# Performance work log

Measured on AMD Instinct MI355X. Metric: run time of the kernel, lower is better.

The kernel has to match this reference:

```python
import jax, jax.numpy as jnp
import numpy as np

B, L, E, H = 2, 2048, 512, 8
D = E // H  # head_dim = 64


def setup_inputs() -> dict:
    key = jax.random.key(0)
    ks = jax.random.split(key, 12)
    s = 0.02
    return {
        "values": jax.random.normal(ks[0], (B, L, E), jnp.float32),
        "keys": jax.random.normal(ks[1], (B, L, E), jnp.float32),
        "query": jax.random.normal(ks[2], (B, L, E), jnp.float32),
        "mask": jax.random.randint(ks[3], (B, 1, L, L), 0, 2, jnp.int32),
        "Wv": jax.random.normal(ks[4], (E, E), jnp.float32) * s,
        "bv": jax.random.normal(ks[5], (E,), jnp.float32) * s,
        "Wk": jax.random.normal(ks[6], (E, E), jnp.float32) * s,
        "bk": jax.random.normal(ks[7], (E,), jnp.float32) * s,
        "Wq": jax.random.normal(ks[8], (E, E), jnp.float32) * s,
        "bq": jax.random.normal(ks[9], (E,), jnp.float32) * s,
        "Wo": jax.random.normal(ks[10], (E, E), jnp.float32) * s,
        "bo": jax.random.normal(ks[11], (E,), jnp.float32) * s,
    }


def reference(values, keys, query, mask, Wv, bv, Wk, bk, Wq, bq, Wo, bo):
    b, lq = query.shape[0], query.shape[1]
    # torch Linear: y = x @ W.T + b
    v = (values @ Wv.T + bv).reshape(b, -1, H, D)
    k = (keys @ Wk.T + bk).reshape(b, -1, H, D)
    q = (query @ Wq.T + bq).reshape(b, lq, H, D)
    energy = jnp.einsum("bqhd,bkhd->bhqk", q, k)  # [B,H,Lq,Lk]
    # mask applied BEFORE the scale, as in the original
    energy = jnp.where(mask == 0, jnp.float32(-1e20), energy)
    # NOTE: scales by sqrt(embed_size), not sqrt(head_dim) (faithful)
    attn = jax.nn.softmax(energy / jnp.sqrt(jnp.float32(E)), axis=3)
    out = jnp.einsum("bhql,blhd->bqhd", attn, v).reshape(b, lq, E)
    return out @ Wo.T + bo
```

## Files before the change

### kernel.cpp

```cpp
#include <hip/hip_runtime.h>
#include <hip/hip_bf16.h>
#include <math.h>

#define BB 2
#define LL 2048
#define EE 512
#define HH 8
#define DD 64
#define MM (BB * LL)
#define LW (LL / 64)

typedef short bf16x8 __attribute__((ext_vector_type(8)));
typedef float f32x4 __attribute__((ext_vector_type(4)));

#define MFMA16(a, b, c) __builtin_amdgcn_mfma_f32_16x16x32_bf16((a), (b), (c), 0, 0, 0)

#if __has_builtin(__builtin_amdgcn_exp2f)
#define EXP2(x) __builtin_amdgcn_exp2f(x)
#else
#define EXP2(x) exp2f(x)
#endif

#define QSCALE 0.0637587146f

__device__ __forceinline__ void gl2lds16(const __hip_bfloat16* g, __hip_bfloat16* l) {
    __builtin_amdgcn_global_load_lds(
        (const __attribute__((address_space(1))) unsigned int*)(g),
        (__attribute__((address_space(3))) unsigned int*)(l),
        16, 0, 0);
}

__device__ __forceinline__ uint4 cvt8_bf16(const float4 a, const float4 b) {
    union { __hip_bfloat16 h[8]; uint4 u; } t;
    t.h[0] = __float2bfloat16(a.x); t.h[1] = __float2bfloat16(a.y);
    t.h[2] = __float2bfloat16(a.z); t.h[3] = __float2bfloat16(a.w);
    t.h[4] = __float2bfloat16(b.x); t.h[5] = __float2bfloat16(b.y);
    t.h[6] = __float2bfloat16(b.z); t.h[7] = __float2bfloat16(b.w);
    return t.u;
}

struct PrepArgs {
    const float* xsrc[3];
    __hip_bfloat16* xdst[3];
    const float* wsrc[4];
    __hip_bfloat16* wdst[4];
    const int* mask;
    unsigned long long* mbits;
};

__global__ __launch_bounds__(256) void prep(PrepArgs a) {
    const int blk = blockIdx.x;
    if (blk < 3072) {
        const int t = blk >> 10;
        const int i = ((blk & 1023) * 256 + threadIdx.x) * 8;
        const float* s = a.xsrc[t] + i;
        float4 f0 = *(const float4*)(s);
        float4 f1 = *(const float4*)(s + 4);
        *(uint4*)(a.xdst[t] + i) = cvt8_bf16(f0, f1);
    } else if (blk < 3584) {
        const int r = blk - 3072;
        const int t = r >> 7;
        const int i = ((r & 127) * 256 + threadIdx.x) * 8;
        const float* s = a.wsrc[t] + i;
        float4 f0 = *(const float4*)(s);
        float4 f1 = *(const float4*)(s + 4);
        *(uint4*)(a.wdst[t] + i) = cvt8_bf16(f0, f1);
    } else {
        const int mb = blk - 3584;
        #pragma unroll
        for (int r = 0; r < 16; ++r) {
            const size_t idx = ((size_t)mb * 16 + r) * 256 + threadIdx.x;
            const int m = a.mask[idx];
            const unsigned long long w = __ballot(m != 0);
            if ((threadIdx.x & 63) == 0) a.mbits[idx >> 6] = w;
        }
    }
}

struct QKVArgs {
    const __hip_bfloat16* X[3];
    const __hip_bfloat16* W[3];
    const float* bias[3];
    __hip_bfloat16* O[3];
};

__global__ __launch_bounds__(256) void gemm_qkv(QKVArgs p) {
    __shared__ __hip_bfloat16 As[2][2][64][32];
    __shared__ __hip_bfloat16 Bs[2][2][128][32];

    const int z = blockIdx.z;
    const __hip_bfloat16* __restrict__ X = p.X[z];
    const __hip_bfloat16* __restrict__ W = p.W[z];
    const float* __restrict__ bias = p.bias[z];
    __hip_bfloat16* __restrict__ O = p.O[z];

    const int tid = threadIdx.x;
    const int wave = tid >> 6, lane = tid & 63;
    const int l15 = lane & 15, quad = lane >> 4;
    const int wn = wave * 32;
    const int m0 = blockIdx.y * 64, n0 = blockIdx.x * 128;

    const int lr = lane >> 2;
    const int lc = (lane & 3) * 8;
    const __hip_bfloat16* Ax = X + (size_t)(m0 + wave * 16 + lr) * EE + lc;
    const __hip_bfloat16* Bx = W + (size_t)(n0 + wave * 32 + lr) * EE + lc;

    f32x4 acc[4][2] = {};

    #define STAGE_G(buf, k0)                                                   \
        gl2lds16(Ax + (k0),           &As[buf][0][wave * 16][0]);              \
        gl2lds16(Ax + (k0) + 32,      &As[buf][1][wave * 16][0]);              \
        gl2lds16(Bx + (k0),           &Bs[buf][0][wave * 32][0]);              \
        gl2lds16(Bx + (k0) + 32,      &Bs[buf][1][wave * 32][0]);              \
        gl2lds16(Bx + (k0) + 16 * EE,      &Bs[buf][0][wave * 32 + 16][0]);    \
        gl2lds16(Bx + (k0) + 16 * EE + 32, &Bs[buf][1][wave * 32 + 16][0]);

    STAGE_G(0, 0);
    __syncthreads();

    for (int kt = 0; kt < 8; ++kt) {
        const int cur = kt & 1;
        if (kt < 7) { STAGE_G(cur ^ 1, (kt + 1) * 64); }

        #pragma unroll
        for (int c = 0; c < 2; ++c) {
            bf16x8 af[4], bf2[2];
            #pragma unroll
            for (int i = 0; i < 4; ++i)
                af[i] = *(const bf16x8*)&As[cur][c][i * 16 + l15][quad * 8];
            #pragma unroll
            for (int j = 0; j < 2; ++j)
                bf2[j] = *(const bf16x8*)&Bs[cur][c][wn + j * 16 + l15][quad * 8];
            #pragma unroll
            for (int i = 0; i < 4; ++i)
                #pragma unroll
                for (int j = 0; j < 2; ++j)
                    acc[i][j] = MFMA16(af[i], bf2[j], acc[i][j]);
        }
        __syncthreads();
    }

    if (z == 2) {
        #pragma unroll
        for (int i = 0; i < 4; ++i)
            #pragma unroll
            for (int j = 0; j < 2; ++j) {
                const int n = n0 + wn + j * 16 + l15;
                const float bv = bias[n];
                const int h = n >> 6, d = n & 63;
                union { __hip_bfloat16 hh[4]; ushort4 v4; } pk;
                #pragma unroll
                for (int reg = 0; reg < 4; ++reg)
                    pk.hh[reg] = __float2bfloat16(acc[i][j][reg] + bv);
                const int m = m0 + i * 16 + quad * 4;
                const int bb = m >> 11, l = m & 2047;
                *(ushort4*)&O[(((size_t)bb * HH + h) * DD + d) * LL + l] = pk.v4;
            }
    } else {
        const float oscale = (z == 0) ? QSCALE : 1.0f;
        #pragma unroll
        for (int i = 0; i < 4; ++i)
            #pragma unroll
            for (int j = 0; j < 2; ++j) {
                const int n = n0 + wn + j * 16 + l15;
                const float bv = bias[n];
                #pragma unroll
                for (int reg = 0; reg < 4; ++reg) {
                    const int m = m0 + i * 16 + quad * 4 + reg;
                    O[(size_t)m * EE + n] = __float2bfloat16((acc[i][j][reg] + bv) * oscale);
                }
            }
    }
}

__global__ __launch_bounds__(256) void gemm_out(
    const __hip_bfloat16* __restrict__ X, const __hip_bfloat16* __restrict__ W,
    const float* __restrict__ bias, float* __restrict__ C) {
    __shared__ __hip_bfloat16 As[2][2][64][32];
    __shared__ __hip_bfloat16 Bs[2][2][128][32];

    const int tid = threadIdx.x;
    const int wave = tid >> 6, lane = tid & 63;
    const int l15 = lane & 15, quad = lane >> 4;
    const int wn = wave * 32;
    const int m0 = blockIdx.y * 64, n0 = blockIdx.x * 128;

    const int lr = lane >> 2;
    const int lc = (lane & 3) * 8;
    const __hip_bfloat16* Ax = X + (size_t)(m0 + wave * 16 + lr) * EE + lc;
    const __hip_bfloat16* Bx = W + (size_t)(n0 + wave * 32 + lr) * EE + lc;

    f32x4 acc[4][2] = {};

    STAGE_G(0, 0);
    __syncthreads();

    for (int kt = 0; kt < 8; ++kt) {
        const int cur = kt & 1;
        if (kt < 7) { STAGE_G(cur ^ 1, (kt + 1) * 64); }

        #pragma unroll
        for (int c = 0; c < 2; ++c) {
            bf16x8 af[4], bf2[2];
            #pragma unroll
            for (int i = 0; i < 4; ++i)
                af[i] = *(const bf16x8*)&As[cur][c][i * 16 + l15][quad * 8];
            #pragma unroll
            for (int j = 0; j < 2; ++j)
                bf2[j] = *(const bf16x8*)&Bs[cur][c][wn + j * 16 + l15][quad * 8];
            #pragma unroll
            for (int i = 0; i < 4; ++i)
                #pragma unroll
                for (int j = 0; j < 2; ++j)
                    acc[i][j] = MFMA16(af[i], bf2[j], acc[i][j]);
        }
        __syncthreads();
    }

    #pragma unroll
    for (int i = 0; i < 4; ++i)
        #pragma unroll
        for (int j = 0; j < 2; ++j) {
            const int n = n0 + wn + j * 16 + l15;
            const float bv = bias[n];
            #pragma unroll
            for (int reg = 0; reg < 4; ++reg) {
                const int m = m0 + i * 16 + quad * 4 + reg;
                C[(size_t)m * EE + n] = acc[i][j][reg] + bv;
            }
        }
}

__global__ __launch_bounds__(256) void attn_mfma(
    const __hip_bfloat16* __restrict__ Qb, const __hip_bfloat16* __restrict__ Kb,
    const __hip_bfloat16* __restrict__ vtg, const unsigned long long* __restrict__ mbits,
    __hip_bfloat16* __restrict__ Op) {
    __shared__ __hip_bfloat16 Ks[2][64][68];
    __shared__ __hip_bfloat16 Vs[2][64][68];
    __shared__ __hip_bfloat16 Ps[4][16][68];

    const int tid = threadIdx.x;
    const int wave = tid >> 6;
    const int lane = tid & 63;
    const int l15 = lane & 15;
    const int quad = lane >> 4;
    const int b = blockIdx.z;
    const int h = blockIdx.y;
    const int q0 = blockIdx.x * 64;
    const int myq = q0 + wave * 16 + l15;

    const int srow = tid >> 2;
    const int scg = (tid & 3) * 16;

    bf16x8 qf[2];
    {
        const __hip_bfloat16* qrow = Qb + ((size_t)b * LL + myq) * EE + h * DD;
        qf[0] = *(const bf16x8*)(qrow + quad * 8);
        qf[1] = *(const bf16x8*)(qrow + 32 + quad * 8);
    }

    const __hip_bfloat16* kbase = Kb + ((size_t)b * LL + srow) * EE + h * DD + scg;
    const __hip_bfloat16* vbase = vtg + (((size_t)b * HH + h) * DD + srow) * LL + scg;
    const unsigned long long* mrow = mbits + ((size_t)b * LL + myq) * LW;

    f32x4 o[4] = {};
    float lrun = 0.f;

    {
        uint4 k0a = *(const uint4*)(kbase);
        uint4 k0b = *(const uint4*)(kbase + 8);
        uint4 v0a = *(const uint4*)(vbase);
        uint4 v0b = *(const uint4*)(vbase + 8);
        *(uint4*)&Ks[0][srow][scg] = k0a;
        *(uint4*)&Ks[0][srow][scg + 8] = k0b;
        *(uint4*)&Vs[0][srow][scg] = v0a;
        *(uint4*)&Vs[0][srow][scg + 8] = v0b;
    }
    unsigned long long mw_cur = mrow[0];
    __syncthreads();

    for (int t = 0; t < LW; ++t) {
        const int cur = t & 1;
        const int nxt = cur ^ 1;
        const bool more = (t + 1) < LW;

        uint4 ka0, ka1, va0, va1;
        unsigned long long mw_n;
        if (more) {
            const __hip_bfloat16* kn = kbase + (size_t)(t + 1) * 64 * EE;
            const __hip_bfloat16* vn = vbase + (t + 1) * 64;
            ka0 = *(const uint4*)(kn);
            ka1 = *(const uint4*)(kn + 8);
            va0 = *(const uint4*)(vn);
            va1 = *(const uint4*)(vn + 8);
            mw_n = mrow[t + 1];
        }

        f32x4 st[4] = {};
        #pragma unroll
        for (int mt = 0; mt < 4; ++mt) {
            bf16x8 a0 = *(const bf16x8*)&Ks[cur][mt * 16 + l15][quad * 8];
            bf16x8 a1 = *(const bf16x8*)&Ks[cur][mt * 16 + l15][32 + quad * 8];
            st[mt] = MFMA16(a0, qf[0], st[mt]);
            st[mt] = MFMA16(a1, qf[1], st[mt]);
        }

        #pragma unroll
        for (int mt = 0; mt < 4; ++mt) {
            float p[4];
            #pragma unroll
            for (int reg = 0; reg < 4; ++reg) {
                const bool live = (mw_cur >> (mt * 16 + quad * 4 + reg)) & 1ull;
                const float e = EXP2(st[mt][reg]);
                p[reg] = live ? e : 0.f;
                lrun += p[reg];
            }
            union { __hip_bfloat162 h2[2]; ushort4 v; } pk;
            pk.h2[0] = __float22bfloat162_rn(make_float2(p[0], p[1]));
            pk.h2[1] = __float22bfloat162_rn(make_float2(p[2], p[3]));
            *(ushort4*)&Ps[wave][l15][mt * 16 + quad * 4] = pk.v;
        }

        bf16x8 pa0 = *(const bf16x8*)&Ps[wave][l15][quad * 8];
        bf16x8 pa1 = *(const bf16x8*)&Ps[wave][l15][32 + quad * 8];
        #pragma unroll
        for (int nt = 0; nt < 4; ++nt) {
            bf16x8 vb0 = *(const bf16x8*)&Vs[cur][nt * 16 + l15][quad * 8];
            bf16x8 vb1 = *(const bf16x8*)&Vs[cur][nt * 16 + l15][32 + quad * 8];
            o[nt] = MFMA16(pa0, vb0, o[nt]);
            o[nt] = MFMA16(pa1, vb1, o[nt]);
        }

        if (more) {
            *(uint4*)&Ks[nxt][srow][scg] = ka0;
            *(uint4*)&Ks[nxt][srow][scg + 8] = ka1;
            *(uint4*)&Vs[nxt][srow][scg] = va0;
            *(uint4*)&Vs[nxt][srow][scg + 8] = va1;
            mw_cur = mw_n;
        }
        __syncthreads();
    }

    lrun += __shfl_xor(lrun, 16);
    lrun += __shfl_xor(lrun, 32);
    const float linv = 1.f / lrun;
    float linvR[4];
    #pragma unroll
    for (int reg = 0; reg < 4; ++reg)
        linvR[reg] = __shfl(linv, quad * 4 + reg);

    __hip_bfloat16* Ob = Op + ((size_t)b * LL + q0 + wave * 16) * EE + h * DD;
    #pragma unroll
    for (int nt = 0; nt < 4; ++nt)
        #pragma unroll
        for (int reg = 0; reg < 4; ++reg) {
            const int qrow = quad * 4 + reg;
            Ob[(size_t)qrow * EE + nt * 16 + l15] =
                __float2bfloat16(o[nt][reg] * linvR[reg]);
        }
}

extern "C" void kernel_launch(void* const* d_in, const int* in_sizes, int n_in,
                              void* d_out, int out_size, void* d_ws, size_t ws_size,
                              hipStream_t stream) {
    const float* values = (const float*)d_in[0];
    const float* keys   = (const float*)d_in[1];
    const float* query  = (const float*)d_in[2];
    const int*   mask   = (const int*)d_in[3];
    const float* Wv = (const float*)d_in[4];
    const float* bv = (const float*)d_in[5];
    const float* Wk = (const float*)d_in[6];
    const float* bk = (const float*)d_in[7];
    const float* Wq = (const float*)d_in[8];
    const float* bq = (const float*)d_in[9];
    const float* Wo = (const float*)d_in[10];
    const float* bo = (const float*)d_in[11];
    float* out = (float*)d_out;

    const size_t XS = (size_t)MM * EE * 2;
    const size_t WS = (size_t)EE * EE * 2;
    char* w = (char*)d_ws;
    __hip_bfloat16* xq  = (__hip_bfloat16*)(w);
    __hip_bfloat16* xk  = (__hip_bfloat16*)(w + XS);
    __hip_bfloat16* xv  = (__hip_bfloat16*)(w + 2 * XS);
    __hip_bfloat16* qb  = (__hip_bfloat16*)(w + 3 * XS);
    __hip_bfloat16* kb  = (__hip_bfloat16*)(w + 4 * XS);
    __hip_bfloat16* vtg = (__hip_bfloat16*)(w + 5 * XS);
    __hip_bfloat16* aob = (__hip_bfloat16*)(w + 6 * XS);
    __hip_bfloat16* wqb = (__hip_bfloat16*)(w + 7 * XS);
    __hip_bfloat16* wkb = (__hip_bfloat16*)(w + 7 * XS + WS);
    __hip_bfloat16* wvb = (__hip_bfloat16*)(w + 7 * XS + 2 * WS);
    __hip_bfloat16* wob = (__hip_bfloat16*)(w + 7 * XS + 3 * WS);
    unsigned long long* mbits = (unsigned long long*)(w + 7 * XS + 4 * WS);

    PrepArgs pa;
    pa.xsrc[0] = query; pa.xsrc[1] = keys; pa.xsrc[2] = values;
    pa.xdst[0] = xq;    pa.xdst[1] = xk;   pa.xdst[2] = xv;
    pa.wsrc[0] = Wq; pa.wsrc[1] = Wk; pa.wsrc[2] = Wv; pa.wsrc[3] = Wo;
    pa.wdst[0] = wqb; pa.wdst[1] = wkb; pa.wdst[2] = wvb; pa.wdst[3] = wob;
    pa.mask = mask; pa.mbits = mbits;

    QKVArgs qa;
    qa.X[0] = xq;  qa.X[1] = xk;  qa.X[2] = xv;
    qa.W[0] = wqb; qa.W[1] = wkb; qa.W[2] = wvb;
    qa.bias[0] = bq; qa.bias[1] = bk; qa.bias[2] = bv;
    qa.O[0] = qb;  qa.O[1] = kb;  qa.O[2] = vtg;

    prep<<<5632, 256, 0, stream>>>(pa);
    gemm_qkv<<<dim3(EE / 128, MM / 64, 3), 256, 0, stream>>>(qa);
    attn_mfma<<<dim3(LL / 64, HH, BB), 256, 0, stream>>>(qb, kb, vtg, mbits, aob);
    gemm_out<<<dim3(EE / 128, MM / 64), 256, 0, stream>>>(aob, wob, bo, out);
}
```

Baseline: 186.3 us.

## Fuse fp32-to-bf16 conversion and mask packing into projection GEMMs

Removes the separate prep kernel. The QKV and output GEMMs now load fp32 activations and weights directly, convert them to bf16 in registers and stage them into LDS, replacing the async global-to-LDS copies. Mask bit-packing moves into an extra z-slice of the QKV grid. The attention kernel now computes the softmax row sum with an MFMA against a ones vector instead of scalar adds and shuffles. This saves one launch and the bf16 round trip through memory. In exchange, the GEMMs redundantly reread fp32 data (twice the bytes, re-read by several tiles), do their conversions inside the main loop, and the mask z-slice blocks carry a heavier serial load each.

```diff
diff --git a/kernel.cpp b/kernel.cpp
--- a/kernel.cpp
+++ b/kernel.cpp
@@ -22,13 +22,6 @@
 #endif
 
 #define QSCALE 0.0637587146f
-
-__device__ __forceinline__ void gl2lds16(const __hip_bfloat16* g, __hip_bfloat16* l) {
-    __builtin_amdgcn_global_load_lds(
-        (const __attribute__((address_space(1))) unsigned int*)(g),
-        (__attribute__((address_space(3))) unsigned int*)(l),
-        16, 0, 0);
-}
 
 __device__ __forceinline__ uint4 cvt8_bf16(const float4 a, const float4 b) {
     union { __hip_bfloat16 h[8]; uint4 u; } t;
@@ -39,88 +32,83 @@
     return t.u;
 }
 
-struct PrepArgs {
-    const float* xsrc[3];
-    __hip_bfloat16* xdst[3];
-    const float* wsrc[4];
-    __hip_bfloat16* wdst[4];
+struct QKVArgs {
+    const float* X[3];
+    const float* W[3];
+    const float* bias[3];
+    __hip_bfloat16* O[3];
     const int* mask;
     unsigned long long* mbits;
 };
 
-__global__ __launch_bounds__(256) void prep(PrepArgs a) {
-    const int blk = blockIdx.x;
-    if (blk < 3072) {
-        const int t = blk >> 10;
-        const int i = ((blk & 1023) * 256 + threadIdx.x) * 8;
-        const float* s = a.xsrc[t] + i;
-        float4 f0 = *(const float4*)(s);
-        float4 f1 = *(const float4*)(s + 4);
-        *(uint4*)(a.xdst[t] + i) = cvt8_bf16(f0, f1);
-    } else if (blk < 3584) {
-        const int r = blk - 3072;
-        const int t = r >> 7;
-        const int i = ((r & 127) * 256 + threadIdx.x) * 8;
-        const float* s = a.wsrc[t] + i;
-        float4 f0 = *(const float4*)(s);
-        float4 f1 = *(const float4*)(s + 4);
-        *(uint4*)(a.wdst[t] + i) = cvt8_bf16(f0, f1);
-    } else {
-        const int mb = blk - 3584;
-        #pragma unroll
-        for (int r = 0; r < 16; ++r) {
-            const size_t idx = ((size_t)mb * 16 + r) * 256 + threadIdx.x;
-            const int m = a.mask[idx];
+__global__ __launch_bounds__(256) void qkv_prep(QKVArgs p) {
+    const int z = blockIdx.z;
+    const int tid = threadIdx.x;
+
+    if (z == 3) {
+        const int mb = blockIdx.y * 4 + blockIdx.x;
+        #pragma unroll 4
+        for (int r = 0; r < 128; ++r) {
+            const size_t idx = ((size_t)mb * 128 + r) * 256 + tid;
+            const int m = p.mask[idx];
             const unsigned long long w = __ballot(m != 0);
-            if ((threadIdx.x & 63) == 0) a.mbits[idx >> 6] = w;
-        }
-    }
-}
-
-struct QKVArgs {
-    const __hip_bfloat16* X[3];
-    const __hip_bfloat16* W[3];
-    const float* bias[3];
-    __hip_bfloat16* O[3];
-};
-
-__global__ __launch_bounds__(256) void gemm_qkv(QKVArgs p) {
+            if ((tid & 63) == 0) p.mbits[idx >> 6] = w;
+        }
+        return;
+    }
+
     __shared__ __hip_bfloat16 As[2][2][64][32];
     __shared__ __hip_bfloat16 Bs[2][2][128][32];
 
-    const int z = blockIdx.z;
-    const __hip_bfloat16* __restrict__ X = p.X[z];
-    const __hip_bfloat16* __restrict__ W = p.W[z];
+    const float* __restrict__ X = p.X[z];
+    const float* __restrict__ W = p.W[z];
     const float* __restrict__ bias = p.bias[z];
     __hip_bfloat16* __restrict__ O = p.O[z];
 
-    const int tid = threadIdx.x;
     const int wave = tid >> 6, lane = tid & 63;
     const int l15 = lane & 15, quad = lane >> 4;
     const int wn = wave * 32;
     const int m0 = blockIdx.y * 64, n0 = blockIdx.x * 128;
 
-    const int lr = lane >> 2;
-    const int lc = (lane & 3) * 8;
-    const __hip_bfloat16* Ax = X + (size_t)(m0 + wave * 16 + lr) * EE + lc;
-    const __hip_bfloat16* Bx = W + (size_t)(n0 + wave * 32 + lr) * EE + lc;
+    const int arow = tid >> 2, acg = (tid & 3) * 16;
+    const int ah = acg >> 5, ac = acg & 31;
+    const int brow = tid >> 1, bcg = (tid & 1) * 32;
+    const int bh = bcg >> 5;
+    const float* Ax = X + (size_t)(m0 + arow) * EE + acg;
+    const float* Bx = W + (size_t)(n0 + brow) * EE + bcg;
 
     f32x4 acc[4][2] = {};
-
-    #define STAGE_G(buf, k0)                                                   \
-        gl2lds16(Ax + (k0),           &As[buf][0][wave * 16][0]);              \
-        gl2lds16(Ax + (k0) + 32,      &As[buf][1][wave * 16][0]);              \
-        gl2lds16(Bx + (k0),           &Bs[buf][0][wave * 32][0]);              \
-        gl2lds16(Bx + (k0) + 32,      &Bs[buf][1][wave * 32][0]);              \
-        gl2lds16(Bx + (k0) + 16 * EE,      &Bs[buf][0][wave * 32 + 16][0]);    \
-        gl2lds16(Bx + (k0) + 16 * EE + 32, &Bs[buf][1][wave * 32 + 16][0]);
-
-    STAGE_G(0, 0);
+    float4 ar[4], br[8];
+
+    #define LOADR(k0)                                                          \
+        ar[0] = *(const float4*)(Ax + (k0));                                   \
+        ar[1] = *(const float4*)(Ax + (k0) + 4);                               \
+        ar[2] = *(const float4*)(Ax + (k0) + 8);                               \
+        ar[3] = *(const float4*)(Ax + (k0) + 12);                              \
+        br[0] = *(const float4*)(Bx + (k0));                                   \
+        br[1] = *(const float4*)(Bx + (k0) + 4);                               \
+        br[2] = *(const float4*)(Bx + (k0) + 8);                               \
+        br[3] = *(const float4*)(Bx + (k0) + 12);                              \
+        br[4] = *(const float4*)(Bx + (k0) + 16);                              \
+        br[5] = *(const float4*)(Bx + (k0) + 20);                              \
+        br[6] = *(const float4*)(Bx + (k0) + 24);                              \
+        br[7] = *(const float4*)(Bx + (k0) + 28);
+
+    #define COMMITR(buf)                                                       \
+        *(uint4*)&As[buf][ah][arow][ac]      = cvt8_bf16(ar[0], ar[1]);        \
+        *(uint4*)&As[buf][ah][arow][ac + 8]  = cvt8_bf16(ar[2], ar[3]);        \
+        *(uint4*)&Bs[buf][bh][brow][0]       = cvt8_bf16(br[0], br[1]);        \
+        *(uint4*)&Bs[buf][bh][brow][8]       = cvt8_bf16(br[2], br[3]);        \
+        *(uint4*)&Bs[buf][bh][brow][16]      = cvt8_bf16(br[4], br[5]);        \
+        *(uint4*)&Bs[buf][bh][brow][24]      = cvt8_bf16(br[6], br[7]);
+
+    LOADR(0);
+    COMMITR(0);
     __syncthreads();
 
     for (int kt = 0; kt < 8; ++kt) {
         const int cur = kt & 1;
-        if (kt < 7) { STAGE_G(cur ^ 1, (kt + 1) * 64); }
+        if (kt < 7) { LOADR((kt + 1) * 64); }
 
         #pragma unroll
         for (int c = 0; c < 2; ++c) {
@@ -137,6 +125,7 @@
                 for (int j = 0; j < 2; ++j)
                     acc[i][j] = MFMA16(af[i], bf2[j], acc[i][j]);
         }
+        if (kt < 7) { COMMITR(cur ^ 1); }
         __syncthreads();
     }
 
@@ -174,7 +163,7 @@
 }
 
 __global__ __launch_bounds__(256) void gemm_out(
-    const __hip_bfloat16* __restrict__ X, const __hip_bfloat16* __restrict__ W,
+    const __hip_bfloat16* __restrict__ X, const float* __restrict__ W,
     const float* __restrict__ bias, float* __restrict__ C) {
     __shared__ __hip_bfloat16 As[2][2][64][32];
     __shared__ __hip_bfloat16 Bs[2][2][128][32];
@@ -185,19 +174,44 @@
     const int wn = wave * 32;
     const int m0 = blockIdx.y * 64, n0 = blockIdx.x * 128;
 
-    const int lr = lane >> 2;
-    const int lc = (lane & 3) * 8;
-    const __hip_bfloat16* Ax = X + (size_t)(m0 + wave * 16 + lr) * EE + lc;
-    const __hip_bfloat16* Bx = W + (size_t)(n0 + wave * 32 + lr) * EE + lc;
+    const int arow = tid >> 2, acg = (tid & 3) * 16;
+    const int ah = acg >> 5, ac = acg & 31;
+    const int brow = tid >> 1, bcg = (tid & 1) * 32;
+    const int bh = bcg >> 5;
+    const __hip_bfloat16* Ax = X + (size_t)(m0 + arow) * EE + acg;
+    const float* Bx = W + (size_t)(n0 + brow) * EE + bcg;
 
     f32x4 acc[4][2] = {};
-
-    STAGE_G(0, 0);
+    uint4 au[2];
+    float4 br[8];
+
+    #define LOADO(k0)                                                          \
+        au[0] = *(const uint4*)(Ax + (k0));                                    \
+        au[1] = *(const uint4*)(Ax + (k0) + 8);                                \
+        br[0] = *(const float4*)(Bx + (k0));                                   \
+        br[1] = *(const float4*)(Bx + (k0) + 4);                               \
+        br[2] = *(const float4*)(Bx + (k0) + 8);                               \
+        br[3] = *(const float4*)(Bx + (k0) + 12);                              \
+        br[4] = *(const float4*)(Bx + (k0) + 16);                              \
+        br[5] = *(const float4*)(Bx + (k0) + 20);                              \
+        br[6] = *(const float4*)(Bx + (k0) + 24);                              \
+        br[7] = *(const float4*)(Bx + (k0) + 28);
+
+    #define COMMITO(buf)                                                       \
+        *(uint4*)&As[buf][ah][arow][ac]     = au[0];                           \
+        *(uint4*)&As[buf][ah][arow][ac + 8] = au[1];                           \
+        *(uint4*)&Bs[buf][bh][brow][0]      = cvt8_bf16(br[0], br[1]);         \
+        *(uint4*)&Bs[buf][bh][brow][8]      = cvt8_bf16(br[2], br[3]);         \
+        *(uint4*)&Bs[buf][bh][brow][16]     = cvt8_bf16(br[4], br[5]);         \
+        *(uint4*)&Bs[buf][bh][brow][24]     = cvt8_bf16(br[6], br[7]);
+
+    LOADO(0);
+    COMMITO(0);
     __syncthreads();
 
     for (int kt = 0; kt < 8; ++kt) {
         const int cur = kt & 1;
-        if (kt < 7) { STAGE_G(cur ^ 1, (kt + 1) * 64); }
+        if (kt < 7) { LOADO((kt + 1) * 64); }
 
         #pragma unroll
         for (int c = 0; c < 2; ++c) {
@@ -214,6 +228,7 @@
                 for (int j = 0; j < 2; ++j)
                     acc[i][j] = MFMA16(af[i], bf2[j], acc[i][j]);
         }
+        if (kt < 7) { COMMITO(cur ^ 1); }
         __syncthreads();
     }
 
@@ -259,12 +274,16 @@
         qf[1] = *(const bf16x8*)(qrow + 32 + quad * 8);
     }
 
+    bf16x8 ones8;
+    #pragma unroll
+    for (int e = 0; e < 8; ++e) ones8[e] = (short)0x3F80;
+
     const __hip_bfloat16* kbase = Kb + ((size_t)b * LL + srow) * EE + h * DD + scg;
     const __hip_bfloat16* vbase = vtg + (((size_t)b * HH + h) * DD + srow) * LL + scg;
     const unsigned long long* mrow = mbits + ((size_t)b * LL + myq) * LW;
 
     f32x4 o[4] = {};
-    float lrun = 0.f;
+    f32x4 o4 = {};
 
     {
         uint4 k0a = *(const uint4*)(kbase);
@@ -307,17 +326,16 @@
 
         #pragma unroll
         for (int mt = 0; mt < 4; ++mt) {
-            float p[4];
+            float pr[4];
             #pragma unroll
             for (int reg = 0; reg < 4; ++reg) {
                 const bool live = (mw_cur >> (mt * 16 + quad * 4 + reg)) & 1ull;
                 const float e = EXP2(st[mt][reg]);
-                p[reg] = live ? e : 0.f;
-                lrun += p[reg];
+                pr[reg] = live ? e : 0.f;
             }
             union { __hip_bfloat162 h2[2]; ushort4 v; } pk;
-            pk.h2[0] = __float22bfloat162_rn(make_float2(p[0], p[1]));
-            pk.h2[1] = __float22bfloat162_rn(make_float2(p[2], p[3]));
+            pk.h2[0] = __float22bfloat162_rn(make_float2(pr[0], pr[1]));
+            pk.h2[1] = __float22bfloat162_rn(make_float2(pr[2], pr[3]));
             *(ushort4*)&Ps[wave][l15][mt * 16 + quad * 4] = pk.v;
         }
 
@@ -330,6 +348,8 @@
             o[nt] = MFMA16(pa0, vb0, o[nt]);
             o[nt] = MFMA16(pa1, vb1, o[nt]);
         }
+        o4 = MFMA16(pa0, ones8, o4);
+        o4 = MFMA16(pa1, ones8, o4);
 
         if (more) {
             *(uint4*)&Ks[nxt][srow][scg] = ka0;
@@ -341,13 +361,10 @@
         __syncthreads();
     }
 
-    lrun += __shfl_xor(lrun, 16);
-    lrun += __shfl_xor(lrun, 32);
-    const float linv = 1.f / lrun;
     float linvR[4];
     #pragma unroll
     for (int reg = 0; reg < 4; ++reg)
-        linvR[reg] = __shfl(linv, quad * 4 + reg);
+        linvR[reg] = 1.f / o4[reg];
 
     __hip_bfloat16* Ob = Op + ((size_t)b * LL + q0 + wave * 16) * EE + h * DD;
     #pragma unroll
@@ -378,36 +395,21 @@
     float* out = (float*)d_out;
 
     const size_t XS = (size_t)MM * EE * 2;
-    const size_t WS = (size_t)EE * EE * 2;
     char* w = (char*)d_ws;
-    __hip_bfloat16* xq  = (__hip_bfloat16*)(w);
-    __hip_bfloat16* xk  = (__hip_bfloat16*)(w + XS);
-    __hip_bfloat16* xv  = (__hip_bfloat16*)(w + 2 * XS);
-    __hip_bfloat16* qb  = (__hip_bfloat16*)(w + 3 * XS);
-    __hip_bfloat16* kb  = (__hip_bfloat16*)(w + 4 * XS);
-    __hip_bfloat16* vtg = (__hip_bfloat16*)(w + 5 * XS);
-    __hip_bfloat16* aob = (__hip_bfloat16*)(w + 6 * XS);
-    __hip_bfloat16* wqb = (__hip_bfloat16*)(w + 7 * XS);
-    __hip_bfloat16* wkb = (__hip_bfloat16*)(w + 7 * XS + WS);
-    __hip_bfloat16* wvb = (__hip_bfloat16*)(w + 7 * XS + 2 * WS);
-    __hip_bfloat16* wob = (__hip_bfloat16*)(w + 7 * XS + 3 * WS);
-    unsigned long long* mbits = (unsigned long long*)(w + 7 * XS + 4 * WS);
-
-    PrepArgs pa;
-    pa.xsrc[0] = query; pa.xsrc[1] = keys; pa.xsrc[2] = values;
-    pa.xdst[0] = xq;    pa.xdst[1] = xk;   pa.xdst[2] = xv;
-    pa.wsrc[0] = Wq; pa.wsrc[1] = Wk; pa.wsrc[2] = Wv; pa.wsrc[3] = Wo;
-    pa.wdst[0] = wqb; pa.wdst[1] = wkb; pa.wdst[2] = wvb; pa.wdst[3] = wob;
-    pa.mask = mask; pa.mbits = mbits;
+    __hip_bfloat16* qb  = (__hip_bfloat16*)(w);
+    __hip_bfloat16* kb  = (__hip_bfloat16*)(w + XS);
+    __hip_bfloat16* vtg = (__hip_bfloat16*)(w + 2 * XS);
+    __hip_bfloat16* aob = (__hip_bfloat16*)(w + 3 * XS);
+    unsigned long long* mbits = (unsigned long long*)(w + 4 * XS);
 
     QKVArgs qa;
-    qa.X[0] = xq;  qa.X[1] = xk;  qa.X[2] = xv;
-    qa.W[0] = wqb; qa.W[1] = wkb; qa.W[2] = wvb;
+    qa.X[0] = query; qa.X[1] = keys; qa.X[2] = values;
+    qa.W[0] = Wq;    qa.W[1] = Wk;   qa.W[2] = Wv;
     qa.bias[0] = bq; qa.bias[1] = bk; qa.bias[2] = bv;
-    qa.O[0] = qb;  qa.O[1] = kb;  qa.O[2] = vtg;
-
-    prep<<<5632, 256, 0, stream>>>(pa);
-    gemm_qkv<<<dim3(EE / 128, MM / 64, 3), 256, 0, stream>>>(qa);
+    qa.O[0] = qb;    qa.O[1] = kb;   qa.O[2] = vtg;
+    qa.mask = mask;  qa.mbits = mbits;
+
+    qkv_prep<<<dim3(EE / 128, MM / 64, 4), 256, 0, stream>>>(qa);
     attn_mfma<<<dim3(LL / 64, HH, BB), 256, 0, stream>>>(qb, kb, vtg, mbits, aob);
-    gemm_out<<<dim3(EE / 128, MM / 64), 256, 0, stream>>>(aob, wob, bo, out);
+    gemm_out<<<dim3(EE / 128, MM / 64), 256, 0, stream>>>(aob, Wo, bo, out);
 }
```

Result: slower. 247.4 us (+32.8%).
